# Kernel optimization log

Hardware: AMD Instinct MI355X
Metric: run time of the kernel (lower is better)

The kernel has to match this reference:

```python
import jax, jax.numpy as jnp
import numpy as np

GRID_SIZE = 5
SPLINE_ORDER = 3
GRID_RANGE = (-1.0, 1.0)
LAYERS = [1024, 1024, 1024]
BATCH = 8192
LN_EPS = 1e-5


def _make_grid(in_features):
    h = (GRID_RANGE[1] - GRID_RANGE[0]) / GRID_SIZE
    n = GRID_SIZE + 2 * SPLINE_ORDER + 1  # 12 knots
    g = jnp.linspace(GRID_RANGE[0] - h * SPLINE_ORDER,
                     GRID_RANGE[1] + h * SPLINE_ORDER, n, dtype=jnp.float32)
    return jnp.broadcast_to(g, (in_features, n))


def setup_inputs() -> dict:
    key = jax.random.key(0)
    ks = jax.random.split(key, 8)
    n_layers = len(LAYERS) - 1
    d_in, d_out = LAYERS[0], LAYERS[1]  # square layers -> stackable params
    coeff = GRID_SIZE + SPLINE_ORDER  # 8
    # kaiming_uniform_(nonlinearity='linear'): bound = sqrt(3) * (1/sqrt(fan_in))
    bw_bound = float(np.sqrt(3.0) / np.sqrt(d_in))
    sw_bound = float(np.sqrt(3.0) / np.sqrt(d_in * coeff))
    x = jax.random.normal(ks[0], (BATCH, d_in), dtype=jnp.float32)
    base_w = jax.random.uniform(ks[1], (n_layers, d_out, d_in), jnp.float32, -bw_bound, bw_bound)
    spline_w = jax.random.uniform(ks[2], (n_layers, d_out, d_in, coeff), jnp.float32, -sw_bound, sw_bound)
    ln_g = jnp.ones((n_layers, d_out), jnp.float32)
    ln_b = jnp.zeros((n_layers, d_out), jnp.float32)
    prelu_a = jnp.full((n_layers,), 0.25, jnp.float32)
    grid = jnp.stack([_make_grid(d_in) for _ in range(n_layers)])  # [L, in, 12]
    return {"x": x, "base_w": base_w, "spline_w": spline_w,
            "ln_g": ln_g, "ln_b": ln_b, "prelu_a": prelu_a, "grid": grid}


def _bspline_bases(x, g):
    """Cox-de Boor recursion. x: [B, in], g: [in, n_knots] -> [B, in, G+order]."""
    xu = x[..., None]  # [B, in, 1]
    bases = ((xu >= g[:, :-1]) & (xu < g[:, 1:])).astype(x.dtype)  # [B, in, 11]
    for k in range(1, SPLINE_ORDER + 1):
        left = g[:, :-(k + 1)]
        right = g[:, k:-1]
        delta = jnp.where(right == left, jnp.ones_like(right), right - left)
        bases = ((xu - left) / delta * bases[..., :-1]
                 + (g[:, k + 1:] - xu) / (g[:, k + 1:] - g[:, 1:-k]) * bases[..., 1:])
    return bases  # [B, in, 8]


def kan_forward(x, base_w, spline_w, ln_g, ln_b, prelu_a, grid):
    n_layers = base_w.shape[0]
    for i in range(n_layers):
        base_out = jnp.matmul(jax.nn.gelu(x, approximate=False), base_w[i].T)  # [B, out]
        bases = _bspline_bases(x, grid[i])  # [B, in, 8]
        spline_out = jnp.matmul(bases.reshape(x.shape[0], -1),
                                spline_w[i].reshape(spline_w.shape[1], -1).T)  # [B, out]
        h = base_out + spline_out
        mu = jnp.mean(h, axis=-1, keepdims=True)
        var = jnp.var(h, axis=-1, keepdims=True)  # biased, matches torch LayerNorm
        h = (h - mu) * jax.lax.rsqrt(var + LN_EPS) * ln_g[i] + ln_b[i]
        x = jnp.where(h >= 0, h, prelu_a[i] * h)  # PReLU (scalar slope per layer)
    return x


def reference(x, base_w, spline_w, ln_g, ln_b, prelu_a, grid):
    return kan_forward(x, base_w, spline_w, ln_g, ln_b, prelu_a, grid)
```

## Files before the change

### kernel.cpp

```cpp
#include <hip/hip_runtime.h>
#include <hip/hip_bf16.h>
#include <cstdint>
#include <cstddef>

typedef __bf16 bf16_t;
typedef __bf16 bf16x8 __attribute__((ext_vector_type(8)));
typedef __bf16 bf16x4 __attribute__((ext_vector_type(4)));
typedef float  f32x4  __attribute__((ext_vector_type(4)));

#define DIM    1024
#define NCOEF  8
#define KTOT   (DIM + DIM * NCOEF)
#define NKNOT  12
#define BATCH  8192
#define LN_EPS 1e-5f

__device__ __forceinline__ float gelu_exact(float x) {
    return 0.5f * x * (1.0f + erff(x * 0.70710678118654752440f));
}

__global__ void pack_w(const float* __restrict__ bw, const float* __restrict__ sw,
                       bf16_t* __restrict__ W) {
    int idx = blockIdx.x * 256 + threadIdx.x;
    bf16_t* wrow = W + (size_t)(idx >> 10) * KTOT;
    int j = idx & 1023;
    wrow[j] = (bf16_t)bw[idx];
    const float4* sp = (const float4*)(sw + (size_t)idx * NCOEF);
    float4 s0 = sp[0], s1 = sp[1];
    bf16x8 v;
    v[0] = (bf16_t)s0.x; v[1] = (bf16_t)s0.y; v[2] = (bf16_t)s0.z; v[3] = (bf16_t)s0.w;
    v[4] = (bf16_t)s1.x; v[5] = (bf16_t)s1.y; v[6] = (bf16_t)s1.z; v[7] = (bf16_t)s1.w;
    *(bf16x8*)(wrow + DIM + j * NCOEF) = v;
}

__global__ void prep_gelu(const float* __restrict__ x, bf16_t* __restrict__ g) {
    int idx = blockIdx.x * 256 + threadIdx.x;
    float4 v = ((const float4*)x)[idx];
    bf16x4 o;
    o[0] = (bf16_t)gelu_exact(v.x); o[1] = (bf16_t)gelu_exact(v.y);
    o[2] = (bf16_t)gelu_exact(v.z); o[3] = (bf16_t)gelu_exact(v.w);
    *(bf16x4*)(g + (size_t)idx * 4) = o;
}

__device__ __forceinline__ void gl_lds16(const void* g, void* l) {
    __builtin_amdgcn_global_load_lds(
        (const __attribute__((address_space(1))) unsigned int*)(uintptr_t)g,
        (__attribute__((address_space(3))) unsigned int*)(uintptr_t)l, 16, 0, 0);
}

__device__ __forceinline__ uint64_t pack4bf(float a, float b, float c, float d) {
    union { bf16_t h[4]; uint64_t q; } u;
    u.h[0] = (bf16_t)a; u.h[1] = (bf16_t)b; u.h[2] = (bf16_t)c; u.h[3] = (bf16_t)d;
    return u.q;
}

__device__ __forceinline__ void spline8(float x, float g0, float invh,
                                        uint64_t& lo, uint64_t& hi) {
    float u = (x - g0) * invh;
    float jf = floorf(u);
    int j = (int)jf;
    float f = u - jf;
    float f2 = f * f, f3 = f2 * f;
    float om = 1.0f - f, om2 = om * om;
    float w0 = om2 * om * (1.0f / 6.0f);
    float w3 = f3 * (1.0f / 6.0f);
    float w1 = fmaf(0.5f, f3, 2.0f / 3.0f) - f2;
    float w2 = 1.0f - w0 - w1 - w3;
    uint64_t W64 = pack4bf(w0, w1, w2, w3);
    if (!(u >= 0.0f && u < 11.0f)) W64 = 0;
    int sh = (j - 3) * 16;
    if (sh >= 0) {
        int s = sh & 63;
        uint64_t loW = W64 << s;
        uint64_t hiW = s ? (W64 >> (64 - s)) : 0ull;
        lo = (sh < 64) ? loW : 0ull;
        hi = (sh < 64) ? hiW : loW;
    } else {
        lo = W64 >> (-sh);
        hi = 0ull;
    }
}

__device__ __forceinline__ void mfma_tile(const bf16_t* __restrict__ Ar0,
                                          const bf16_t* __restrict__ Ar1,
                                          const bf16_t* __restrict__ Br0,
                                          const bf16_t* __restrict__ Br1,
                                          f32x4 (&acc)[4][4]) {
#pragma unroll
    for (int kk = 0; kk < 2; kk++) {
        const bf16_t* Ar = kk ? Ar1 : Ar0;
        const bf16_t* Br = kk ? Br1 : Br0;
        bf16x8 af[4], bfr[4];
#pragma unroll
        for (int i = 0; i < 4; i++) af[i] = *(const bf16x8*)(Ar + i * 16 * 64);
#pragma unroll
        for (int j = 0; j < 4; j++) bfr[j] = *(const bf16x8*)(Br + j * 16 * 64);
#pragma unroll
        for (int i = 0; i < 4; i++)
#pragma unroll
            for (int j = 0; j < 4; j++)
                acc[i][j] = __builtin_amdgcn_mfma_f32_16x16x32_bf16(af[i], bfr[j], acc[i][j], 0, 0, 0);
    }
}

__global__ __launch_bounds__(256) void gemm_fused(
    const float* __restrict__ Y,
    const bf16_t* __restrict__ G,
    const bf16_t* __restrict__ W,
    float* __restrict__ C,
    const float* __restrict__ gp,
    int mmask, int mshift) {
    constexpr int K = KTOT, N = DIM;
    __shared__ __align__(16) bf16_t At[64 * 64];
    __shared__ __align__(16) bf16_t Bt[256 * 64];
    const int tid = threadIdx.x;
    const int l = tid & 63;
    const int w = tid >> 6;
    const int bm = blockIdx.x & mmask, bn = blockIdx.x >> mshift;

    const float g0 = gp[0];
    const float invh = 1.0f / (gp[1] - gp[0]);

    const int lrow = tid >> 3;
    const int lchk = (tid & 7) ^ (lrow & 7);
    const bf16_t* Gg = G + (size_t)(bm * 64 + lrow) * DIM + lchk * 8;
    const bf16_t* Bg = W + (size_t)(bn * 256 + lrow) * K + lchk * 8;
    bf16_t* Al = At + tid * 8;
    bf16_t* Bl = Bt + tid * 8;

    const float* Yb = Y + (size_t)(bm * 64 + lrow) * DIM + (tid & 7);
    bf16_t* As = At + lrow * 64 + lchk * 8;

    f32x4 acc[4][4] = {};
    const int cA = (l >> 4) ^ (l & 7);
    const bf16_t* Ar0 = At + (l & 15) * 64 + cA * 8;
    const bf16_t* Ar1 = At + (l & 15) * 64 + (cA ^ 4) * 8;
    const bf16_t* Br0 = Bt + (w * 64 + (l & 15)) * 64 + cA * 8;
    const bf16_t* Br1 = Bt + (w * 64 + (l & 15)) * 64 + (cA ^ 4) * 8;

    for (int k0 = 0; k0 < DIM; k0 += 64) {
#pragma unroll
        for (int q = 0; q < 2; q++)
            gl_lds16(Gg + (size_t)q * 32 * DIM + k0, Al + q * 2048);
#pragma unroll
        for (int q = 0; q < 8; q++)
            gl_lds16(Bg + (size_t)q * 32 * K + k0, Bl + q * 2048);
        asm volatile("s_waitcnt vmcnt(0)" ::: "memory");
        __syncthreads();
        mfma_tile(Ar0, Ar1, Br0, Br1, acc);
        __syncthreads();
    }

    float ycur[2], ynext[2];
#pragma unroll
    for (int q = 0; q < 2; q++) ycur[q] = Yb[(size_t)q * 32 * DIM];

    for (int k0 = DIM; k0 < K; k0 += 64) {
        const int j0 = (k0 - DIM) >> 3;
        const bool more = (k0 + 64) < K;
        if (more) {
#pragma unroll
            for (int q = 0; q < 2; q++) ynext[q] = Yb[(size_t)q * 32 * DIM + j0 + 8];
        }
#pragma unroll
        for (int q = 0; q < 8; q++)
            gl_lds16(Bg + (size_t)q * 32 * K + k0, Bl + q * 2048);
#pragma unroll
        for (int q = 0; q < 2; q++) {
            uint64_t lo, hi;
            spline8(ycur[q], g0, invh, lo, hi);
            union { uint64_t u[2]; uint4 v; } ov;
            ov.u[0] = lo; ov.u[1] = hi;
            *(uint4*)(As + q * 32 * 64) = ov.v;
        }
        asm volatile("s_waitcnt vmcnt(0)" ::: "memory");
        __syncthreads();
        mfma_tile(Ar0, Ar1, Br0, Br1, acc);
        __syncthreads();
        if (more) {
#pragma unroll
            for (int q = 0; q < 2; q++) ycur[q] = ynext[q];
        }
    }

    const int r0 = bm * 64 + (l >> 4) * 4;
    const int c0 = bn * 256 + w * 64 + (l & 15);
#pragma unroll
    for (int i = 0; i < 4; i++)
#pragma unroll
        for (int j = 0; j < 4; j++)
#pragma unroll
            for (int r = 0; r < 4; r++)
                C[(size_t)(r0 + i * 16 + r) * N + c0 + j * 16] = acc[i][j][r];
}

__global__ void ln_mid(const float* __restrict__ h, const float* __restrict__ g_ln,
                       const float* __restrict__ b_ln, const float* __restrict__ pa,
                       float* __restrict__ y, bf16_t* __restrict__ yg) {
    const int row = blockIdx.x, tid = threadIdx.x;
    const int w = tid >> 6, l = tid & 63;
    f32x4 v = *(const f32x4*)(h + (size_t)row * DIM + tid * 4);
    float s = v[0] + v[1] + v[2] + v[3];
    float q = v[0] * v[0] + v[1] * v[1] + v[2] * v[2] + v[3] * v[3];
#pragma unroll
    for (int o = 32; o > 0; o >>= 1) { s += __shfl_xor(s, o); q += __shfl_xor(q, o); }
    __shared__ float rs[4], rq[4];
    if (l == 0) { rs[w] = s; rq[w] = q; }
    __syncthreads();
    s = rs[0] + rs[1] + rs[2] + rs[3];
    q = rq[0] + rq[1] + rq[2] + rq[3];
    float mean = s * (1.0f / DIM);
    float var = q * (1.0f / DIM) - mean * mean;
    float rstd = rsqrtf(var + LN_EPS);
    float a = pa[0];
    f32x4 o4;
    bf16x4 g4;
#pragma unroll
    for (int c = 0; c < 4; c++) {
        int col = tid * 4 + c;
        float yv = (v[c] - mean) * rstd * g_ln[col] + b_ln[col];
        yv = (yv >= 0.0f) ? yv : a * yv;
        o4[c] = yv;
        g4[c] = (bf16_t)gelu_exact(yv);
    }
    *(f32x4*)(y + (size_t)row * DIM + tid * 4) = o4;
    *(bf16x4*)(yg + (size_t)row * DIM + tid * 4) = g4;
}

__global__ void ln_out(const float* __restrict__ h, const float* __restrict__ g_ln,
                       const float* __restrict__ b_ln, const float* __restrict__ pa,
                       float* __restrict__ out) {
    const int row = blockIdx.x, tid = threadIdx.x;
    const int w = tid >> 6, l = tid & 63;
    f32x4 v = *(const f32x4*)(h + (size_t)row * DIM + tid * 4);
    float s = v[0] + v[1] + v[2] + v[3];
    float q = v[0] * v[0] + v[1] * v[1] + v[2] * v[2] + v[3] * v[3];
#pragma unroll
    for (int o = 32; o > 0; o >>= 1) { s += __shfl_xor(s, o); q += __shfl_xor(q, o); }
    __shared__ float rs[4], rq[4];
    if (l == 0) { rs[w] = s; rq[w] = q; }
    __syncthreads();
    s = rs[0] + rs[1] + rs[2] + rs[3];
    q = rq[0] + rq[1] + rq[2] + rq[3];
    float mean = s * (1.0f / DIM);
    float var = q * (1.0f / DIM) - mean * mean;
    float rstd = rsqrtf(var + LN_EPS);
    float a = pa[0];
    f32x4 o4;
#pragma unroll
    for (int c = 0; c < 4; c++) {
        int col = tid * 4 + c;
        float yv = (v[c] - mean) * rstd * g_ln[col] + b_ln[col];
        o4[c] = (yv >= 0.0f) ? yv : a * yv;
    }
    *(f32x4*)(out + (size_t)row * DIM + tid * 4) = o4;
}

extern "C" void kernel_launch(void* const* d_in, const int* in_sizes, int n_in,
                              void* d_out, int out_size, void* d_ws, size_t ws_size,
                              hipStream_t stream) {
    const float* x    = (const float*)d_in[0];
    const float* bw   = (const float*)d_in[1];
    const float* sw   = (const float*)d_in[2];
    const float* ln_g = (const float*)d_in[3];
    const float* ln_b = (const float*)d_in[4];
    const float* pa   = (const float*)d_in[5];
    const float* grid = (const float*)d_in[6];
    float* out = (float*)d_out;

    const size_t wbytes = (size_t)2 * DIM * KTOT * sizeof(bf16_t);
    int R = 8192;
    while (R > 128 && wbytes + (size_t)R * DIM * 10 > ws_size) R >>= 1;
    int mtiles = R / 64;
    int mshift = 0; while ((1 << mshift) < mtiles) mshift++;
    int mmask = mtiles - 1;

    char* wsc = (char*)d_ws;
    bf16_t* Wbuf = (bf16_t*)wsc;
    bf16_t* ygel = (bf16_t*)(wsc + wbytes);
    float*  ybuf = (float*)(wsc + wbytes + (size_t)R * DIM * 2);
    float*  hbuf = (float*)(wsc + wbytes + (size_t)R * DIM * 6);

    pack_w<<<(2 * DIM * DIM) / 256, 256, 0, stream>>>(bw, sw, Wbuf);

    const int nslab = BATCH / R;
    for (int sidx = 0; sidx < nslab; sidx++) {
        const size_t row0 = (size_t)sidx * R;
        const float* x0 = x + row0 * DIM;
        prep_gelu<<<R * DIM / 1024, 256, 0, stream>>>(x0, ygel);
        gemm_fused<<<mtiles * 4, 256, 0, stream>>>(x0, ygel, Wbuf, hbuf,
                                                   grid, mmask, mshift);
        ln_mid<<<R, 256, 0, stream>>>(hbuf, ln_g, ln_b, pa, ybuf, ygel);
        gemm_fused<<<mtiles * 4, 256, 0, stream>>>(ybuf, ygel, Wbuf + (size_t)DIM * KTOT, hbuf,
                                                   grid + DIM * NKNOT, mmask, mshift);
        ln_out<<<R, 256, 0, stream>>>(hbuf, ln_g + DIM, ln_b + DIM, pa + 1, out + row0 * DIM);
    }
}
```

Baseline: 524.3 us.

## Split GEMM K dimension across blocks and reduce partials in LayerNorm

Adds split-K to the fused GEMM. Each block handles half of the combined GELU+spline K range and writes its own partial output slab, and the LayerNorm kernels sum the partial slabs before normalizing. This doubles the number of GEMM blocks to improve CU occupancy and load balance, since with R=8192 there are only 512 output tiles. In exchange it adds extra fp32 partial-output writes and reads and needs more workspace, falling back to KS=1 when the workspace is too small.

```diff
diff --git a/kernel.cpp b/kernel.cpp
--- a/kernel.cpp
+++ b/kernel.cpp
@@ -109,14 +109,19 @@
     const bf16_t* __restrict__ W,
     float* __restrict__ C,
     const float* __restrict__ gp,
-    int mmask, int mshift) {
-    constexpr int K = KTOT, N = DIM;
+    int mmask, int mshift, int ksz, size_t cstride) {
+    constexpr int N = DIM;
     __shared__ __align__(16) bf16_t At[64 * 64];
     __shared__ __align__(16) bf16_t Bt[256 * 64];
     const int tid = threadIdx.x;
     const int l = tid & 63;
     const int w = tid >> 6;
-    const int bm = blockIdx.x & mmask, bn = blockIdx.x >> mshift;
+    const int bm = blockIdx.x & mmask;
+    const int bn = (blockIdx.x >> mshift) & 3;
+    const int ks = blockIdx.x >> (mshift + 2);
+    const int kbeg = ks * ksz, kend = kbeg + ksz;
+    const int kgelu_end = (kend < DIM) ? kend : DIM;
+    const int kspl_beg = (kbeg > DIM) ? kbeg : DIM;
 
     const float g0 = gp[0];
     const float invh = 1.0f / (gp[1] - gp[0]);
@@ -124,7 +129,7 @@
     const int lrow = tid >> 3;
     const int lchk = (tid & 7) ^ (lrow & 7);
     const bf16_t* Gg = G + (size_t)(bm * 64 + lrow) * DIM + lchk * 8;
-    const bf16_t* Bg = W + (size_t)(bn * 256 + lrow) * K + lchk * 8;
+    const bf16_t* Bg = W + (size_t)(bn * 256 + lrow) * KTOT + lchk * 8;
     bf16_t* Al = At + tid * 8;
     bf16_t* Bl = Bt + tid * 8;
 
@@ -138,51 +143,55 @@
     const bf16_t* Br0 = Bt + (w * 64 + (l & 15)) * 64 + cA * 8;
     const bf16_t* Br1 = Bt + (w * 64 + (l & 15)) * 64 + (cA ^ 4) * 8;
 
-    for (int k0 = 0; k0 < DIM; k0 += 64) {
+    for (int k0 = kbeg; k0 < kgelu_end; k0 += 64) {
 #pragma unroll
         for (int q = 0; q < 2; q++)
             gl_lds16(Gg + (size_t)q * 32 * DIM + k0, Al + q * 2048);
 #pragma unroll
         for (int q = 0; q < 8; q++)
-            gl_lds16(Bg + (size_t)q * 32 * K + k0, Bl + q * 2048);
+            gl_lds16(Bg + (size_t)q * 32 * KTOT + k0, Bl + q * 2048);
         asm volatile("s_waitcnt vmcnt(0)" ::: "memory");
         __syncthreads();
         mfma_tile(Ar0, Ar1, Br0, Br1, acc);
         __syncthreads();
     }
 
-    float ycur[2], ynext[2];
-#pragma unroll
-    for (int q = 0; q < 2; q++) ycur[q] = Yb[(size_t)q * 32 * DIM];
-
-    for (int k0 = DIM; k0 < K; k0 += 64) {
-        const int j0 = (k0 - DIM) >> 3;
-        const bool more = (k0 + 64) < K;
-        if (more) {
-#pragma unroll
-            for (int q = 0; q < 2; q++) ynext[q] = Yb[(size_t)q * 32 * DIM + j0 + 8];
+    if (kspl_beg < kend) {
+        float ycur[2], ynext[2];
+        const int jbase = (kspl_beg - DIM) >> 3;
+#pragma unroll
+        for (int q = 0; q < 2; q++) ycur[q] = Yb[(size_t)q * 32 * DIM + jbase];
+
+        for (int k0 = kspl_beg; k0 < kend; k0 += 64) {
+            const int j0 = (k0 - DIM) >> 3;
+            const bool more = (k0 + 64) < kend;
+            if (more) {
+#pragma unroll
+                for (int q = 0; q < 2; q++) ynext[q] = Yb[(size_t)q * 32 * DIM + j0 + 8];
+            }
+#pragma unroll
+            for (int q = 0; q < 8; q++)
+                gl_lds16(Bg + (size_t)q * 32 * KTOT + k0, Bl + q * 2048);
+#pragma unroll
+            for (int q = 0; q < 2; q++) {
+                uint64_t lo, hi;
+                spline8(ycur[q], g0, invh, lo, hi);
+                union { uint64_t u[2]; uint4 v; } ov;
+                ov.u[0] = lo; ov.u[1] = hi;
+                *(uint4*)(As + q * 32 * 64) = ov.v;
+            }
+            asm volatile("s_waitcnt vmcnt(0)" ::: "memory");
+            __syncthreads();
+            mfma_tile(Ar0, Ar1, Br0, Br1, acc);
+            __syncthreads();
+            if (more) {
+#pragma unroll
+                for (int q = 0; q < 2; q++) ycur[q] = ynext[q];
+            }
         }
-#pragma unroll
-        for (int q = 0; q < 8; q++)
-            gl_lds16(Bg + (size_t)q * 32 * K + k0, Bl + q * 2048);
-#pragma unroll
-        for (int q = 0; q < 2; q++) {
-            uint64_t lo, hi;
-            spline8(ycur[q], g0, invh, lo, hi);
-            union { uint64_t u[2]; uint4 v; } ov;
-            ov.u[0] = lo; ov.u[1] = hi;
-            *(uint4*)(As + q * 32 * 64) = ov.v;
-        }
-        asm volatile("s_waitcnt vmcnt(0)" ::: "memory");
-        __syncthreads();
-        mfma_tile(Ar0, Ar1, Br0, Br1, acc);
-        __syncthreads();
-        if (more) {
-#pragma unroll
-            for (int q = 0; q < 2; q++) ycur[q] = ynext[q];
-        }
-    }
-
+    }
+
+    float* Cs = C + (size_t)ks * cstride;
     const int r0 = bm * 64 + (l >> 4) * 4;
     const int c0 = bn * 256 + w * 64 + (l & 15);
 #pragma unroll
@@ -191,15 +200,20 @@
         for (int j = 0; j < 4; j++)
 #pragma unroll
             for (int r = 0; r < 4; r++)
-                C[(size_t)(r0 + i * 16 + r) * N + c0 + j * 16] = acc[i][j][r];
+                Cs[(size_t)(r0 + i * 16 + r) * N + c0 + j * 16] = acc[i][j][r];
 }
 
 __global__ void ln_mid(const float* __restrict__ h, const float* __restrict__ g_ln,
                        const float* __restrict__ b_ln, const float* __restrict__ pa,
-                       float* __restrict__ y, bf16_t* __restrict__ yg) {
+                       float* __restrict__ y, bf16_t* __restrict__ yg,
+                       int nks, size_t cstride) {
     const int row = blockIdx.x, tid = threadIdx.x;
     const int w = tid >> 6, l = tid & 63;
     f32x4 v = *(const f32x4*)(h + (size_t)row * DIM + tid * 4);
+    for (int s = 1; s < nks; s++) {
+        f32x4 v2 = *(const f32x4*)(h + s * cstride + (size_t)row * DIM + tid * 4);
+        v[0] += v2[0]; v[1] += v2[1]; v[2] += v2[2]; v[3] += v2[3];
+    }
     float s = v[0] + v[1] + v[2] + v[3];
     float q = v[0] * v[0] + v[1] * v[1] + v[2] * v[2] + v[3] * v[3];
 #pragma unroll
@@ -229,10 +243,14 @@
 
 __global__ void ln_out(const float* __restrict__ h, const float* __restrict__ g_ln,
                        const float* __restrict__ b_ln, const float* __restrict__ pa,
-                       float* __restrict__ out) {
+                       float* __restrict__ out, int nks, size_t cstride) {
     const int row = blockIdx.x, tid = threadIdx.x;
     const int w = tid >> 6, l = tid & 63;
     f32x4 v = *(const f32x4*)(h + (size_t)row * DIM + tid * 4);
+    for (int s = 1; s < nks; s++) {
+        f32x4 v2 = *(const f32x4*)(h + s * cstride + (size_t)row * DIM + tid * 4);
+        v[0] += v2[0]; v[1] += v2[1]; v[2] += v2[2]; v[3] += v2[3];
+    }
     float s = v[0] + v[1] + v[2] + v[3];
     float q = v[0] * v[0] + v[1] * v[1] + v[2] * v[2] + v[3] * v[3];
 #pragma unroll
@@ -269,11 +287,19 @@
     float* out = (float*)d_out;
 
     const size_t wbytes = (size_t)2 * DIM * KTOT * sizeof(bf16_t);
+    int KS = 2;
     int R = 8192;
-    while (R > 128 && wbytes + (size_t)R * DIM * 10 > ws_size) R >>= 1;
+    auto need = [&](int r, int k) {
+        return wbytes + (size_t)r * DIM * (size_t)(6 + 4 * k);
+    };
+    if (need(8192, 2) > ws_size) KS = 1;
+    while (R > 128 && need(R, KS) > ws_size) R >>= 1;
+    const int ksz = KTOT / KS;
+
     int mtiles = R / 64;
     int mshift = 0; while ((1 << mshift) < mtiles) mshift++;
     int mmask = mtiles - 1;
+    const size_t cstride = (size_t)R * DIM;
 
     char* wsc = (char*)d_ws;
     bf16_t* Wbuf = (bf16_t*)wsc;
@@ -288,11 +314,11 @@
         const size_t row0 = (size_t)sidx * R;
         const float* x0 = x + row0 * DIM;
         prep_gelu<<<R * DIM / 1024, 256, 0, stream>>>(x0, ygel);
-        gemm_fused<<<mtiles * 4, 256, 0, stream>>>(x0, ygel, Wbuf, hbuf,
-                                                   grid, mmask, mshift);
-        ln_mid<<<R, 256, 0, stream>>>(hbuf, ln_g, ln_b, pa, ybuf, ygel);
-        gemm_fused<<<mtiles * 4, 256, 0, stream>>>(ybuf, ygel, Wbuf + (size_t)DIM * KTOT, hbuf,
-                                                   grid + DIM * NKNOT, mmask, mshift);
-        ln_out<<<R, 256, 0, stream>>>(hbuf, ln_g + DIM, ln_b + DIM, pa + 1, out + row0 * DIM);
-    }
-}
+        gemm_fused<<<mtiles * 4 * KS, 256, 0, stream>>>(x0, ygel, Wbuf, hbuf,
+                                                        grid, mmask, mshift, ksz, cstride);
+        ln_mid<<<R, 256, 0, stream>>>(hbuf, ln_g, ln_b, pa, ybuf, ygel, KS, cstride);
+        gemm_fused<<<mtiles * 4 * KS, 256, 0, stream>>>(ybuf, ygel, Wbuf + (size_t)DIM * KTOT, hbuf,
+                                                        grid + DIM * NKNOT, mmask, mshift, ksz, cstride);
+        ln_out<<<R, 256, 0, stream>>>(hbuf, ln_g + DIM, ln_b + DIM, pa + 1, out + row0 * DIM, KS, cstride);
+    }
+}
```

New measurement: 555.7 us. 6.0% more time.
